# Kernel optimization log

Measured on AMD Instinct MI355X. Metric: run time of the kernel, lower is better.

## Reference

```python
import jax, jax.numpy as jnp
import numpy as np


def setup_inputs() -> dict:
    key = jax.random.key(0)
    k1, k2, k3 = jax.random.split(key, 3)
    B, C, S, D = 8, 256, 2048, 64
    a = jax.random.normal(k1, (B, C, S), dtype=jnp.float32)
    b = jax.random.normal(k2, (B, S, D), dtype=jnp.float32)
    c = jax.random.normal(k3, (B, S, D), dtype=jnp.float32)
    return {"a": a, "b": b, "c": c}


def reference(a, b, c):
    # mid[b, n, m] = softmax_m(b @ c^T), unscaled
    scores = jnp.einsum("bnd,bmd->bnm", b, c)
    mid = jax.nn.softmax(scores, axis=-1)  # [B, S, S]
    # out = a @ mid^T + a  -> [B, C, S]
    out = jnp.einsum("bcm,bnm->bcn", a, mid) + a
    return out
```

## Files before the change

kernel.cpp:

```cpp
#include <hip/hip_runtime.h>
#include <stdint.h>

#define S 2048
#define DHEAD 64
#define CDIM 256
#define NBATCH 8
#define NMT 16

typedef __attribute__((ext_vector_type(4))) float f32x4;
typedef __attribute__((ext_vector_type(8))) short s16x8;
typedef __attribute__((ext_vector_type(8))) _Float16 f16x8;
typedef __attribute__((ext_vector_type(4))) unsigned short u16x4;

static __device__ __forceinline__ unsigned short f2bf(float f) {
    unsigned int u = __builtin_bit_cast(unsigned int, f);
    unsigned int r = (u + 0x7FFFu + ((u >> 16) & 1u)) >> 16;
    return (unsigned short)r;
}
static __device__ __forceinline__ unsigned short f2h(float f) {
    _Float16 h = (_Float16)f;
    return __builtin_bit_cast(unsigned short, h);
}
static __device__ __forceinline__ float bf2f(unsigned short u) {
    return __builtin_bit_cast(float, (unsigned int)u << 16);
}

#define GLOAD16(g, l)                                                              \
    __builtin_amdgcn_global_load_lds(                                              \
        (const __attribute__((address_space(1))) void*)(g),                        \
        (__attribute__((address_space(3))) void*)(l), 16, 0, 0)

__global__ __launch_bounds__(256) void cvt_kernel(
    const float* __restrict__ a, const float* __restrict__ b, const float* __restrict__ c,
    unsigned short* __restrict__ a16, unsigned short* __restrict__ b16,
    unsigned short* __restrict__ c16)
{
    const int na4 = NBATCH * CDIM * S / 4;
    const int nbc4 = NBATCH * S * DHEAD / 4;
    int i0 = blockIdx.x * 256 + threadIdx.x;
    int stride = gridDim.x * 256;
    for (int i = i0; i < na4; i += stride) {
        f32x4 v = ((const f32x4*)a)[i];
        u16x4 o; o.x = f2bf(v.x); o.y = f2bf(v.y); o.z = f2bf(v.z); o.w = f2bf(v.w);
        ((u16x4*)a16)[i] = o;
    }
    for (int i = i0; i < nbc4; i += stride) {
        f32x4 v = ((const f32x4*)b)[i];
        u16x4 o; o.x = f2h(v.x); o.y = f2h(v.y); o.z = f2h(v.z); o.w = f2h(v.w);
        ((u16x4*)b16)[i] = o;
        f32x4 u = ((const f32x4*)c)[i];
        u16x4 p; p.x = f2h(u.x); p.y = f2h(u.y); p.z = f2h(u.z); p.w = f2h(u.w);
        ((u16x4*)c16)[i] = p;
    }
}

__global__ __launch_bounds__(256) void scores_kernel(
    const unsigned short* __restrict__ B16, const unsigned short* __restrict__ C16,
    unsigned short* __restrict__ E, float* __restrict__ Lp, int b0, int nb)
{
    const int bid = blockIdx.x;
    int lb, idx;
    if (nb == 8) { lb = bid & 7; idx = bid >> 3; }
    else { lb = bid / (NMT * 16); idx = bid - lb * (NMT * 16); }
    const int gb = b0 + lb;
    const int mt = idx & 15;
    const int m0 = mt * 128;
    const int n0 = (idx >> 4) * 128;
    const unsigned short* __restrict__ bp = B16 + (size_t)gb * S * DHEAD;
    const unsigned short* __restrict__ cp = C16 + (size_t)gb * S * DHEAD;
    unsigned short* __restrict__ Ep = E + (size_t)lb * S * S;

    extern __shared__ char smem[];
    unsigned short* cs = (unsigned short*)smem;
    unsigned short* bs = cs + 128 * 64;
    unsigned short* es = (unsigned short*)smem;
    float* Lsh = (float*)(smem + 34816);

    const int tid = threadIdx.x;
    const int lane = tid & 63;
    const int w = tid >> 6;
    const int wr = w >> 1, wc = w & 1;
    const int q = lane >> 4, r15 = lane & 15;

    #pragma unroll
    for (int t = 0; t < 4; ++t) {
        int r = w + 4 * t;
        int ch = r * 64 + lane;
        int row = ch >> 3;
        int off = ((ch & 7) ^ (row & 7)) * 8;
        GLOAD16(cp + (size_t)(m0 + row) * DHEAD + off, &cs[r * 512]);
        GLOAD16(bp + (size_t)(n0 + row) * DHEAD + off, &bs[r * 512]);
    }
    __syncthreads();

    f32x4 acc[4][4] = {};
    #pragma unroll
    for (int kk = 0; kk < 2; ++kk) {
        const int sz = ((kk * 4 + q) ^ (r15 & 7)) * 8;
        f16x8 af[4], bf[4];
        #pragma unroll
        for (int i = 0; i < 4; ++i)
            af[i] = *(const f16x8*)&cs[(wr * 64 + i * 16 + r15) * 64 + sz];
        #pragma unroll
        for (int j = 0; j < 4; ++j)
            bf[j] = *(const f16x8*)&bs[(wc * 64 + j * 16 + r15) * 64 + sz];
        #pragma unroll
        for (int i = 0; i < 4; ++i)
            #pragma unroll
            for (int j = 0; j < 4; ++j)
                acc[i][j] = __builtin_amdgcn_mfma_f32_16x16x32_f16(af[i], bf[j], acc[i][j], 0, 0, 0);
    }

    u16x4 pk[4][4];
    float sj[4] = {0.f, 0.f, 0.f, 0.f};
    #pragma unroll
    for (int i = 0; i < 4; ++i) {
        #pragma unroll
        for (int j = 0; j < 4; ++j) {
            float e0 = __expf(acc[i][j][0]);
            float e1 = __expf(acc[i][j][1]);
            float e2 = __expf(acc[i][j][2]);
            float e3 = __expf(acc[i][j][3]);
            pk[i][j].x = f2bf(e0); pk[i][j].y = f2bf(e1);
            pk[i][j].z = f2bf(e2); pk[i][j].w = f2bf(e3);
            sj[j] += (e0 + e1) + (e2 + e3);
        }
    }
    #pragma unroll
    for (int j = 0; j < 4; ++j) {
        sj[j] += __shfl_xor(sj[j], 16);
        sj[j] += __shfl_xor(sj[j], 32);
    }

    __syncthreads();

    #pragma unroll
    for (int i = 0; i < 4; ++i)
        #pragma unroll
        for (int j = 0; j < 4; ++j) {
            int nl = wc * 64 + j * 16 + r15;
            int ml = wr * 64 + i * 16 + q * 4;
            *(u16x4*)&es[nl * 136 + ml] = pk[i][j];
        }
    if (q == 0) {
        #pragma unroll
        for (int j = 0; j < 4; ++j)
            Lsh[wr * 128 + wc * 64 + j * 16 + r15] = sj[j];
    }
    __syncthreads();

    if (tid < 128)
        Lp[(size_t)lb * NMT * S + (size_t)mt * S + n0 + tid] = Lsh[tid] + Lsh[128 + tid];

    #pragma unroll
    for (int t = 0; t < 8; ++t) {
        int ch = tid + 256 * t;
        int row = ch >> 4, off = ch & 15;
        f32x4 v = *(const f32x4*)&es[row * 136 + off * 8];
        *(f32x4*)&Ep[(size_t)(n0 + row) * S + m0 + off * 8] = v;
    }
}

__global__ __launch_bounds__(256, 2) void gemm_kernel(
    const unsigned short* __restrict__ a16, const unsigned short* __restrict__ E,
    const float* __restrict__ Lp, float* __restrict__ out, int b0, int nb)
{
    const int bid = blockIdx.x;
    int lb, idx;
    if (nb == 8) { lb = bid & 7; idx = bid >> 3; }
    else { lb = bid / 64; idx = bid - lb * 64; }
    const int gb = b0 + lb;
    const int nt = idx >> 1, ct = idx & 1;
    const int n0 = nt * 64, c0 = ct * 128;

    const unsigned short* __restrict__ Ap = a16 + (size_t)gb * CDIM * S;
    const unsigned short* __restrict__ Bp = E + (size_t)lb * S * S;
    float* __restrict__ op = out + (size_t)gb * CDIM * S;

    __shared__ unsigned short As[2][128 * 64];
    __shared__ unsigned short Bs[2][64 * 64];

    const int tid = threadIdx.x;
    const int lane = tid & 63;
    const int w = tid >> 6;
    const int wr = w >> 1, wc = w & 1;
    const int q = lane >> 4, r15 = lane & 15;

    int aRow[4], aOff[4], aR_[4], bRow[2], bOff[2], bR_[2];
    #pragma unroll
    for (int t = 0; t < 4; ++t) {
        int r = w + 4 * t, ch = r * 64 + lane;
        aR_[t] = r; aRow[t] = ch >> 3;
        aOff[t] = ((ch & 7) ^ ((ch >> 3) & 7)) * 8;
    }
    #pragma unroll
    for (int t = 0; t < 2; ++t) {
        int r = w + 4 * t, ch = r * 64 + lane;
        bR_[t] = r; bRow[t] = ch >> 3;
        bOff[t] = ((ch & 7) ^ ((ch >> 3) & 7)) * 8;
    }

#define STAGE(buf, k0)                                                            \
    {                                                                             \
        _Pragma("unroll")                                                         \
        for (int t = 0; t < 4; ++t)                                               \
            GLOAD16(Ap + (size_t)(c0 + aRow[t]) * S + (k0) + aOff[t],             \
                    &As[buf][aR_[t] * 512]);                                      \
        _Pragma("unroll")                                                         \
        for (int t = 0; t < 2; ++t)                                               \
            GLOAD16(Bp + (size_t)(n0 + bRow[t]) * S + (k0) + bOff[t],             \
                    &Bs[buf][bR_[t] * 512]);                                      \
    }

    f32x4 acc[4][2] = {};

    STAGE(0, 0);
    __syncthreads();

    const int sw0 = (q ^ (r15 & 7)) * 8;
    const int sw1 = ((4 + q) ^ (r15 & 7)) * 8;

    #pragma unroll 2
    for (int kt = 0; kt < S / 64; ++kt) {
        const int cur = kt & 1;
        if (kt < S / 64 - 1) STAGE(cur ^ 1, (kt + 1) * 64);

        #pragma unroll
        for (int kk = 0; kk < 2; ++kk) {
            const int sz = kk ? sw1 : sw0;
            s16x8 af[4], bf[2];
            #pragma unroll
            for (int i = 0; i < 4; ++i)
                af[i] = *(const s16x8*)&As[cur][(wr * 64 + i * 16 + r15) * 64 + sz];
            #pragma unroll
            for (int j = 0; j < 2; ++j)
                bf[j] = *(const s16x8*)&Bs[cur][(wc * 32 + j * 16 + r15) * 64 + sz];
            #pragma unroll
            for (int i = 0; i < 4; ++i)
                #pragma unroll
                for (int j = 0; j < 2; ++j)
                    acc[i][j] = __builtin_amdgcn_mfma_f32_16x16x32_bf16(af[i], bf[j], acc[i][j], 0, 0, 0);
        }
        __syncthreads();
    }
#undef STAGE

    float rcpL[2];
    #pragma unroll
    for (int j = 0; j < 2; ++j) {
        int n = n0 + wc * 32 + j * 16 + r15;
        float s = 0.f;
        #pragma unroll
        for (int mt = 0; mt < NMT; ++mt)
            s += Lp[(size_t)lb * NMT * S + (size_t)mt * S + n];
        rcpL[j] = 1.0f / s;
    }
    #pragma unroll
    for (int i = 0; i < 4; ++i) {
        #pragma unroll
        for (int rr = 0; rr < 4; ++rr) {
            int cc = c0 + wr * 64 + i * 16 + q * 4 + rr;
            size_t base = (size_t)cc * S;
            #pragma unroll
            for (int j = 0; j < 2; ++j) {
                int n = n0 + wc * 32 + j * 16 + r15;
                op[base + n] = acc[i][j][rr] * rcpL[j] + bf2f(Ap[base + n]);
            }
        }
    }
}

extern "C" void kernel_launch(void* const* d_in, const int* in_sizes, int n_in,
                              void* d_out, int out_size, void* d_ws, size_t ws_size,
                              hipStream_t stream) {
    const float* a = (const float*)d_in[0];
    const float* b = (const float*)d_in[1];
    const float* c = (const float*)d_in[2];
    float* out = (float*)d_out;

    const size_t a16_bytes = (size_t)NBATCH * CDIM * S * 2;
    const size_t bc_bytes = (size_t)NBATCH * S * DHEAD * 2;
    const size_t head = a16_bytes + 2 * bc_bytes;
    const size_t perb = (size_t)S * S * 2 + (size_t)NMT * S * 4;
    int G = 1;
    if (ws_size > head + perb) {
        size_t g = (ws_size - head) / perb;
        G = (g >= NBATCH) ? NBATCH : (int)g;
        if (G < 1) G = 1;
    }
    unsigned short* a16 = (unsigned short*)d_ws;
    unsigned short* b16 = (unsigned short*)((char*)d_ws + a16_bytes);
    unsigned short* c16 = (unsigned short*)((char*)d_ws + a16_bytes + bc_bytes);
    unsigned short* E = (unsigned short*)((char*)d_ws + head);
    float* Lp = (float*)((char*)d_ws + head + (size_t)G * S * S * 2);

    cvt_kernel<<<1024, 256, 0, stream>>>(a, b, c, a16, b16, c16);

    const size_t lds1 = 34816 + 2 * 128 * 4;
    for (int b0 = 0; b0 < NBATCH; b0 += G) {
        int nb = (NBATCH - b0 < G) ? (NBATCH - b0) : G;
        scores_kernel<<<NMT * 16 * nb, 256, lds1, stream>>>(b16, c16, E, Lp, b0, nb);
        gemm_kernel<<<64 * nb, 256, 0, stream>>>(a16, E, Lp, out, b0, nb);
    }
}
```

Measured before the change: 61.54 us.

## Triple-buffer the output GEMM with explicit vmcnt waits and raw barriers

Replaces the double-buffered GEMM main loop with a three-stage LDS ring in dynamic shared memory. Global-to-LDS loads run two K-tiles ahead, and completion is tracked with explicit s_waitcnt vmcnt counts plus raw s_barrier instead of __syncthreads. MFMA issue is raised with s_setprio. The aim is to hide global load latency better, at the cost of 72KB of LDS per block, which may limit the two-blocks-per-CU occupancy, and the hand-counted vmcnt values are fragile. If the dynamic LDS attribute cannot be set, the old kernel is kept as a fallback.

Result: faster. 50.62 us (-17.7%).

```diff
diff --git a/kernel.cpp b/kernel.cpp
--- a/kernel.cpp
+++ b/kernel.cpp
@@ -6,6 +6,7 @@
 #define CDIM 256
 #define NBATCH 8
 #define NMT 16
+#define NSTEP 32
 
 typedef __attribute__((ext_vector_type(4))) float f32x4;
 typedef __attribute__((ext_vector_type(8))) short s16x8;
@@ -161,7 +162,64 @@
     }
 }
 
-__global__ __launch_bounds__(256, 2) void gemm_kernel(
+#define GEMM_DECODE()                                                             \
+    const int tid = threadIdx.x;                                                  \
+    const int lane = tid & 63;                                                    \
+    const int w = tid >> 6;                                                       \
+    const int wr = w >> 1, wc = w & 1;                                            \
+    const int q = lane >> 4, r15 = lane & 15;                                     \
+    int aRow[4], aOff[4], aR_[4], bRow[2], bOff[2], bR_[2];                       \
+    _Pragma("unroll")                                                             \
+    for (int t = 0; t < 4; ++t) {                                                 \
+        int r = w + 4 * t, ch = r * 64 + lane;                                    \
+        aR_[t] = r; aRow[t] = ch >> 3;                                            \
+        aOff[t] = ((ch & 7) ^ ((ch >> 3) & 7)) * 8;                               \
+    }                                                                             \
+    _Pragma("unroll")                                                             \
+    for (int t = 0; t < 2; ++t) {                                                 \
+        int r = w + 4 * t, ch = r * 64 + lane;                                    \
+        bR_[t] = r; bRow[t] = ch >> 3;                                            \
+        bOff[t] = ((ch & 7) ^ ((ch >> 3) & 7)) * 8;                               \
+    }
+
+#define STAGEP(bufA, bufB, k0)                                                    \
+    {                                                                             \
+        _Pragma("unroll")                                                         \
+        for (int t = 0; t < 4; ++t)                                               \
+            GLOAD16(Ap + (size_t)(c0 + aRow[t]) * S + (k0) + aOff[t],             \
+                    (bufA) + aR_[t] * 512);                                       \
+        _Pragma("unroll")                                                         \
+        for (int t = 0; t < 2; ++t)                                               \
+            GLOAD16(Bp + (size_t)(n0 + bRow[t]) * S + (k0) + bOff[t],             \
+                    (bufB) + bR_[t] * 512);                                       \
+    }
+
+#define GEMM_EPILOGUE()                                                           \
+    float rcpL[2];                                                                \
+    _Pragma("unroll")                                                             \
+    for (int j = 0; j < 2; ++j) {                                                 \
+        int n = n0 + wc * 32 + j * 16 + r15;                                      \
+        float s = 0.f;                                                            \
+        _Pragma("unroll")                                                         \
+        for (int mt = 0; mt < NMT; ++mt)                                          \
+            s += Lp[(size_t)lb * NMT * S + (size_t)mt * S + n];                   \
+        rcpL[j] = 1.0f / s;                                                       \
+    }                                                                             \
+    _Pragma("unroll")                                                             \
+    for (int i = 0; i < 4; ++i) {                                                 \
+        _Pragma("unroll")                                                         \
+        for (int rr = 0; rr < 4; ++rr) {                                          \
+            int cc = c0 + wr * 64 + i * 16 + q * 4 + rr;                          \
+            size_t base = (size_t)cc * S;                                         \
+            _Pragma("unroll")                                                     \
+            for (int j = 0; j < 2; ++j) {                                         \
+                int n = n0 + wc * 32 + j * 16 + r15;                              \
+                op[base + n] = acc[i][j][rr] * rcpL[j] + bf2f(Ap[base + n]);      \
+            }                                                                     \
+        }                                                                         \
+    }
+
+__global__ __launch_bounds__(256, 2) void gemm_kernel3(
     const unsigned short* __restrict__ a16, const unsigned short* __restrict__ E,
     const float* __restrict__ Lp, float* __restrict__ out, int b0, int nb)
 {
@@ -177,97 +235,122 @@
     const unsigned short* __restrict__ Bp = E + (size_t)lb * S * S;
     float* __restrict__ op = out + (size_t)gb * CDIM * S;
 
-    __shared__ unsigned short As[2][128 * 64];
-    __shared__ unsigned short Bs[2][64 * 64];
-
-    const int tid = threadIdx.x;
-    const int lane = tid & 63;
-    const int w = tid >> 6;
-    const int wr = w >> 1, wc = w & 1;
-    const int q = lane >> 4, r15 = lane & 15;
-
-    int aRow[4], aOff[4], aR_[4], bRow[2], bOff[2], bR_[2];
-    #pragma unroll
-    for (int t = 0; t < 4; ++t) {
-        int r = w + 4 * t, ch = r * 64 + lane;
-        aR_[t] = r; aRow[t] = ch >> 3;
-        aOff[t] = ((ch & 7) ^ ((ch >> 3) & 7)) * 8;
-    }
-    #pragma unroll
-    for (int t = 0; t < 2; ++t) {
-        int r = w + 4 * t, ch = r * 64 + lane;
-        bR_[t] = r; bRow[t] = ch >> 3;
-        bOff[t] = ((ch & 7) ^ ((ch >> 3) & 7)) * 8;
-    }
-
-#define STAGE(buf, k0)                                                            \
-    {                                                                             \
-        _Pragma("unroll")                                                         \
-        for (int t = 0; t < 4; ++t)                                               \
-            GLOAD16(Ap + (size_t)(c0 + aRow[t]) * S + (k0) + aOff[t],             \
-                    &As[buf][aR_[t] * 512]);                                      \
-        _Pragma("unroll")                                                         \
-        for (int t = 0; t < 2; ++t)                                               \
-            GLOAD16(Bp + (size_t)(n0 + bRow[t]) * S + (k0) + bOff[t],             \
-                    &Bs[buf][bR_[t] * 512]);                                      \
-    }
+    extern __shared__ char gsm[];
+    unsigned short* As[3];
+    unsigned short* Bs[3];
+    #pragma unroll
+    for (int u = 0; u < 3; ++u) {
+        As[u] = (unsigned short*)gsm + u * (128 * 64 + 64 * 64);
+        Bs[u] = As[u] + 128 * 64;
+    }
+
+    GEMM_DECODE();
 
     f32x4 acc[4][2] = {};
 
-    STAGE(0, 0);
-    __syncthreads();
+    STAGEP(As[0], Bs[0], 0);
+    STAGEP(As[1], Bs[1], 64);
 
     const int sw0 = (q ^ (r15 & 7)) * 8;
     const int sw1 = ((4 + q) ^ (r15 & 7)) * 8;
 
-    #pragma unroll 2
-    for (int kt = 0; kt < S / 64; ++kt) {
-        const int cur = kt & 1;
-        if (kt < S / 64 - 1) STAGE(cur ^ 1, (kt + 1) * 64);
-
+    #pragma unroll
+    for (int kt = 0; kt < NSTEP; ++kt) {
+        const int cur = kt % 3;
+        if (kt <= NSTEP - 3) {
+            STAGEP(As[(kt + 2) % 3], Bs[(kt + 2) % 3], (kt + 2) * 64);
+            asm volatile("s_waitcnt vmcnt(12)" ::: "memory");
+        } else if (kt == NSTEP - 2) {
+            asm volatile("s_waitcnt vmcnt(6)" ::: "memory");
+        } else {
+            asm volatile("s_waitcnt vmcnt(0)" ::: "memory");
+        }
+        __builtin_amdgcn_sched_barrier(0);
+        __builtin_amdgcn_s_barrier();
+        __builtin_amdgcn_sched_barrier(0);
+
+        const unsigned short* Ar = As[cur];
+        const unsigned short* Br = Bs[cur];
         #pragma unroll
         for (int kk = 0; kk < 2; ++kk) {
             const int sz = kk ? sw1 : sw0;
             s16x8 af[4], bf[2];
             #pragma unroll
             for (int i = 0; i < 4; ++i)
-                af[i] = *(const s16x8*)&As[cur][(wr * 64 + i * 16 + r15) * 64 + sz];
+                af[i] = *(const s16x8*)&Ar[(wr * 64 + i * 16 + r15) * 64 + sz];
             #pragma unroll
             for (int j = 0; j < 2; ++j)
-                bf[j] = *(const s16x8*)&Bs[cur][(wc * 32 + j * 16 + r15) * 64 + sz];
+                bf[j] = *(const s16x8*)&Br[(wc * 32 + j * 16 + r15) * 64 + sz];
+            __builtin_amdgcn_s_setprio(1);
             #pragma unroll
             for (int i = 0; i < 4; ++i)
                 #pragma unroll
                 for (int j = 0; j < 2; ++j)
                     acc[i][j] = __builtin_amdgcn_mfma_f32_16x16x32_bf16(af[i], bf[j], acc[i][j], 0, 0, 0);
+            __builtin_amdgcn_s_setprio(0);
+        }
+
+        __builtin_amdgcn_sched_barrier(0);
+        __builtin_amdgcn_s_barrier();
+    }
+
+    GEMM_EPILOGUE();
+}
+
+__global__ __launch_bounds__(256, 2) void gemm_kernel2(
+    const unsigned short* __restrict__ a16, const unsigned short* __restrict__ E,
+    const float* __restrict__ Lp, float* __restrict__ out, int b0, int nb)
+{
+    const int bid = blockIdx.x;
+    int lb, idx;
+    if (nb == 8) { lb = bid & 7; idx = bid >> 3; }
+    else { lb = bid / 64; idx = bid - lb * 64; }
+    const int gb = b0 + lb;
+    const int nt = idx >> 1, ct = idx & 1;
+    const int n0 = nt * 64, c0 = ct * 128;
+
+    const unsigned short* __restrict__ Ap = a16 + (size_t)gb * CDIM * S;
+    const unsigned short* __restrict__ Bp = E + (size_t)lb * S * S;
+    float* __restrict__ op = out + (size_t)gb * CDIM * S;
+
+    __shared__ unsigned short AsS[2][128 * 64];
+    __shared__ unsigned short BsS[2][64 * 64];
+
+    GEMM_DECODE();
+
+    f32x4 acc[4][2] = {};
+
+    STAGEP(AsS[0], BsS[0], 0);
+    __syncthreads();
+
+    const int sw0 = (q ^ (r15 & 7)) * 8;
+    const int sw1 = ((4 + q) ^ (r15 & 7)) * 8;
+
+    #pragma unroll 2
+    for (int kt = 0; kt < NSTEP; ++kt) {
+        const int cur = kt & 1;
+        if (kt < NSTEP - 1) STAGEP(AsS[cur ^ 1], BsS[cur ^ 1], (kt + 1) * 64);
+
+        #pragma unroll
+        for (int kk = 0; kk < 2; ++kk) {
+            const int sz = kk ? sw1 : sw0;
+            s16x8 af[4], bf[2];
+            #pragma unroll
+            for (int i = 0; i < 4; ++i)
+                af[i] = *(const s16x8*)&AsS[cur][(wr * 64 + i * 16 + r15) * 64 + sz];
+            #pragma unroll
+            for (int j = 0; j < 2; ++j)
+                bf[j] = *(const s16x8*)&BsS[cur][(wc * 32 + j * 16 + r15) * 64 + sz];
+            #pragma unroll
+            for (int i = 0; i < 4; ++i)
+                #pragma unroll
+                for (int j = 0; j < 2; ++j)
+                    acc[i][j] = __builtin_amdgcn_mfma_f32_16x16x32_bf16(af[i], bf[j], acc[i][j], 0, 0, 0);
         }
         __syncthreads();
     }
-#undef STAGE
-
-    float rcpL[2];
-    #pragma unroll
-    for (int j = 0; j < 2; ++j) {
-        int n = n0 + wc * 32 + j * 16 + r15;
-        float s = 0.f;
-        #pragma unroll
-        for (int mt = 0; mt < NMT; ++mt)
-            s += Lp[(size_t)lb * NMT * S + (size_t)mt * S + n];
-        rcpL[j] = 1.0f / s;
-    }
-    #pragma unroll
-    for (int i = 0; i < 4; ++i) {
-        #pragma unroll
-        for (int rr = 0; rr < 4; ++rr) {
-            int cc = c0 + wr * 64 + i * 16 + q * 4 + rr;
-            size_t base = (size_t)cc * S;
-            #pragma unroll
-            for (int j = 0; j < 2; ++j) {
-                int n = n0 + wc * 32 + j * 16 + r15;
-                op[base + n] = acc[i][j][rr] * rcpL[j] + bf2f(Ap[base + n]);
-            }
-        }
-    }
+
+    GEMM_EPILOGUE();
 }
 
 extern "C" void kernel_launch(void* const* d_in, const int* in_sizes, int n_in,
@@ -294,12 +377,20 @@
     unsigned short* E = (unsigned short*)((char*)d_ws + head);
     float* Lp = (float*)((char*)d_ws + head + (size_t)G * S * S * 2);
 
+    const int gemm_lds3 = 3 * (128 * 64 + 64 * 64) * 2;
+    hipError_t attr_ok = hipFuncSetAttribute(
+        reinterpret_cast<const void*>(gemm_kernel3),
+        hipFuncAttributeMaxDynamicSharedMemorySize, gemm_lds3);
+
     cvt_kernel<<<1024, 256, 0, stream>>>(a, b, c, a16, b16, c16);
 
     const size_t lds1 = 34816 + 2 * 128 * 4;
     for (int b0 = 0; b0 < NBATCH; b0 += G) {
         int nb = (NBATCH - b0 < G) ? (NBATCH - b0) : G;
         scores_kernel<<<NMT * 16 * nb, 256, lds1, stream>>>(b16, c16, E, Lp, b0, nb);
-        gemm_kernel<<<64 * nb, 256, 0, stream>>>(a16, E, Lp, out, b0, nb);
-    }
-}
+        if (attr_ok == hipSuccess)
+            gemm_kernel3<<<64 * nb, 256, gemm_lds3, stream>>>(a16, E, Lp, out, b0, nb);
+        else
+            gemm_kernel2<<<64 * nb, 256, 0, stream>>>(a16, E, Lp, out, b0, nb);
+    }
+}
```
